# Kernel tuning notes

Measured on AMD Instinct MI355X. Metric: run time of the kernel, lower is better.

## Reference

```python
import jax, jax.numpy as jnp
import numpy as np

B, D, H, C = 512, 1024, 512, 4


def setup_inputs() -> dict:
    key = jax.random.key(0)
    k_x, k_v, k_w = jax.random.split(key, 3)
    # x holds categorical values in [0, C) used as float multipliers
    x = jax.random.randint(k_x, (B, D), 0, C).astype(jnp.float32)
    # xavier_normal_ per torch fan computation: V fan_in=D*C, fan_out=H*C; W fan_in=D, fan_out=H
    V = jax.random.normal(k_v, (H, D, C), jnp.float32) * np.float32(np.sqrt(2.0 / (D * C + H * C)))
    b = jnp.zeros((D, C), jnp.float32)
    W = jax.random.normal(k_w, (H, D), jnp.float32) * np.float32(np.sqrt(2.0 / (D + H)))
    c = jnp.zeros((1, H), jnp.float32)
    return {"x": x, "V": V, "b": b, "W": W, "c": c}


def _nade_forward(x, V, b, W, c):
    Bsz = x.shape[0]
    a0 = jnp.broadcast_to(c, (Bsz, c.shape[1]))  # [B, H]
    # per-step slices stacked along leading D axis for lax.scan
    xs = (jnp.transpose(V, (1, 0, 2)),  # [D, H, C]
          b,                            # [D, C]
          W.T,                          # [D, H]
          x.T)                          # [D, B]

    def step(a, inp):
        V_d, b_d, w_d, x_d = inp
        h = jax.nn.sigmoid(a)                 # [B, H]
        logits = h @ V_d + b_d                # [B, C]
        p = jax.nn.log_softmax(logits, axis=1)
        a_new = a + x_d[:, None] * w_d[None, :]  # rank-1 update of running preactivation
        return a_new, (logits, p)

    _, (logits, p) = jax.lax.scan(step, a0, xs)   # each [D, B, C]
    y_hat = jnp.transpose(logits, (1, 0, 2)).reshape(Bsz, -1)  # [B, D*C], d-major blocks of size C
    p_hat = jnp.transpose(p, (1, 0, 2)).reshape(Bsz, -1)
    return y_hat, p_hat


def reference(x, V, b, W, c):
    return _nade_forward(x, V, b, W, c)
```

## Files before the change

### kernel.cpp

```cpp
#include <hip/hip_runtime.h>


#define Bv 512
#define Dv 1024
#define Hv 512
#define Cv 4
#define Kv 32
#define DCv 32

#define L2E 1.4426950408889634f
#define LN2 0.6931471805599453f

typedef __attribute__((ext_vector_type(8))) short short8;
typedef __attribute__((ext_vector_type(4))) float f32x4;

__device__ __forceinline__ float fexp2(float x) { return __builtin_amdgcn_exp2f(x); }
__device__ __forceinline__ float flog2(float x) { return __builtin_amdgcn_logf(x); }
__device__ __forceinline__ float frcp(float x)  { return __builtin_amdgcn_rcpf(x); }

__device__ __forceinline__ unsigned bf16pk(float lo, float hi) {
    return __builtin_amdgcn_perm(__float_as_uint(hi), __float_as_uint(lo), 0x07060302u);
}
__device__ __forceinline__ unsigned short bf16rne(float f) {
    unsigned u = __float_as_uint(f);
    return (unsigned short)((u + 0x7FFFu + ((u >> 16) & 1u)) >> 16);
}

__global__ __launch_bounds__(256) void k_prep2(
        const float* __restrict__ W, const float* __restrict__ x,
        const float* __restrict__ V,
        float* __restrict__ WtL, float* __restrict__ xt,
        unsigned short* __restrict__ VtA4) {
    __shared__ __align__(16) char smem[16640];
    const int blk = blockIdx.x;

    if (blk < 1024) {
        unsigned short* tile = (unsigned short*)smem;
        const int d0 = (blk >> 2) * 4;
        const int hq = blk & 3;
        const int dd  = threadIdx.x & 3;
        const int hb0 = threadIdx.x >> 2;
#pragma unroll
        for (int p = 0; p < 2; ++p) {
            int h = hq * 128 + p * 64 + hb0;
            float4 v = *(const float4*)(V + ((size_t)h * Dv + d0 + dd) * Cv);
            int hbl = (h >> 5) - hq * 4;
            int q = (h >> 3) & 3, j = h & 7;
            int base = (dd * 4 + hbl) * 128 + q * 32 + j;
            tile[base + 0 * 8] = bf16rne(v.x);
            tile[base + 1 * 8] = bf16rne(v.y);
            tile[base + 2 * 8] = bf16rne(v.z);
            tile[base + 3 * 8] = bf16rne(v.w);
        }
        __syncthreads();
        {
            const uint4* srcp = (const uint4*)tile;
            int tt  = threadIdx.x;
            int dd2 = tt >> 6;
            int off = tt & 63;
            uint4* dst = (uint4*)VtA4;
            dst[(size_t)(d0 + dd2) * 256 + hq * 64 + off] = srcp[dd2 * 64 + off];
        }
    } else {
        float (*t)[65] = (float(*)[65])smem;
        const int t2   = blk - 1024;
        const int mb   = t2 >> 7;
        const int tile = t2 & 127;
        const int tr   = tile >> 4;
        const int tc   = tile & 15;
        const float* src = mb ? x : W;
        float* dst       = mb ? xt : WtL;
        const float scale = mb ? 1.0f : L2E;
        const int lx = threadIdx.x & 15;
        const int ly = threadIdx.x >> 4;
#pragma unroll
        for (int r = 0; r < 64; r += 16) {
            int row = r + ly;
            float4 v = *(const float4*)(src + (size_t)(tr * 64 + row) * Dv + tc * 64 + lx * 4);
            t[row][lx * 4 + 0] = v.x;
            t[row][lx * 4 + 1] = v.y;
            t[row][lx * 4 + 2] = v.z;
            t[row][lx * 4 + 3] = v.w;
        }
        __syncthreads();
#pragma unroll
        for (int r = 0; r < 64; r += 16) {
            int row = r + ly;
            float4 o = make_float4(t[lx * 4 + 0][row] * scale,
                                   t[lx * 4 + 1][row] * scale,
                                   t[lx * 4 + 2][row] * scale,
                                   t[lx * 4 + 3][row] * scale);
            *(float4*)(dst + (size_t)(tc * 64 + row) * 512 + tr * 64 + lx * 4) = o;
        }
    }
}

__global__ __launch_bounds__(512) void k_partial(const float* __restrict__ x,
                          const float* __restrict__ WtL, float* __restrict__ A0) {
    int k  = blockIdx.x >> 6;
    int bg = blockIdx.x & 63;
    int h  = threadIdx.x;
    int d0 = k * DCv;

    __shared__ float xs[DCv * 8];
    if (threadIdx.x < DCv * 8) {
        int g = threadIdx.x >> 5;
        int j = threadIdx.x & 31;
        xs[j * 8 + g] = x[(size_t)(bg * 8 + g) * Dv + d0 + j];
    }
    __syncthreads();

    float acc[8];
#pragma unroll
    for (int g = 0; g < 8; ++g) acc[g] = 0.0f;

    const float* wp = WtL + (size_t)d0 * Hv + h;
    for (int j = 0; j < DCv; ++j) {
        float wv = wp[(size_t)j * Hv];
        const float4 x0 = *(const float4*)(xs + j * 8);
        const float4 x1 = *(const float4*)(xs + j * 8 + 4);
        acc[0] = fmaf(x0.x, wv, acc[0]);
        acc[1] = fmaf(x0.y, wv, acc[1]);
        acc[2] = fmaf(x0.z, wv, acc[2]);
        acc[3] = fmaf(x0.w, wv, acc[3]);
        acc[4] = fmaf(x1.x, wv, acc[4]);
        acc[5] = fmaf(x1.y, wv, acc[5]);
        acc[6] = fmaf(x1.z, wv, acc[6]);
        acc[7] = fmaf(x1.w, wv, acc[7]);
    }
#pragma unroll
    for (int g = 0; g < 8; ++g)
        A0[((size_t)k * Bv + bg * 8 + g) * Hv + h] = acc[g];
}

__global__ void k_prefix(float* __restrict__ A0, const float* __restrict__ cbias) {
    int gid = blockIdx.x * blockDim.x + threadIdx.x;
    int h = gid & (Hv - 1);
    int bi = gid >> 9;
    float run = cbias[h] * L2E;
    float* p = A0 + (size_t)bi * Hv + h;
    for (int k = 0; k < Kv; ++k) {
        float t = p[(size_t)k * Bv * Hv];
        p[(size_t)k * Bv * Hv] = run;
        run += t;
    }
}

__global__ __launch_bounds__(256, 4) void k_main(
        const float* __restrict__ xt, const float* __restrict__ bbias,
        const unsigned short* __restrict__ VtA4, const float* __restrict__ WtL,
        const float* __restrict__ A0, float* __restrict__ out) {
    const int k    = blockIdx.x >> 5;
    const int bg   = blockIdx.x & 31;
    const int wid  = threadIdx.x >> 6;
    const int lane = threadIdx.x & 63;
    const int bl   = lane & 15;
    const int quad = lane >> 4;
    const int b    = bg * 16 + bl;
    const int d0   = k * DCv;

    __shared__ f32x4 red[2][8][4][16];

    float a[32];
    {
        const float* ap = A0 + ((size_t)k * Bv + b) * Hv + wid * 128 + quad * 8;
#pragma unroll
        for (int kb = 0; kb < 4; ++kb) {
            float4 t0 = *(const float4*)(ap + kb * 32);
            float4 t1 = *(const float4*)(ap + kb * 32 + 4);
            a[kb*8+0]=t0.x; a[kb*8+1]=t0.y; a[kb*8+2]=t0.z; a[kb*8+3]=t0.w;
            a[kb*8+4]=t1.x; a[kb*8+5]=t1.y; a[kb*8+6]=t1.z; a[kb*8+7]=t1.w;
        }
    }

    const bool act = (bl < 4);
    const unsigned short* vp = VtA4 + (((size_t)d0 * 16 + wid * 4) * 16 + quad * 4 + bl) * 8;
    const float* wp = WtL + (size_t)d0 * Hv + wid * 128 + quad * 8;
    const float* xp = xt + (size_t)d0 * Bv + b;

    const int  sE  = wid * 2 + (lane >> 5);
    const bool epi = ((lane >> 4) & 1) == 0;
    const float* bpE = bbias + (d0 + sE) * Cv;
    float* spY = out + (size_t)b * Dv * Cv + (d0 + sE) * Cv;
    float* spP = spY + (size_t)Bv * Dv * Cv;

    const short8 zfrag = {0,0,0,0,0,0,0,0};

    for (int i1 = 0; i1 < DCv / 8; ++i1) {
        const int buf = i1 & 1;
#pragma unroll 1
        for (int half = 0; half < 2; ++half) {
#pragma unroll
            for (int s = 0; s < 4; ++s) {
                short8 af[4];
#pragma unroll
                for (int kb = 0; kb < 4; ++kb)
                    af[kb] = act ? *(const short8*)(vp + s * 2048 + kb * 128) : zfrag;
                float xd = xp[s * Bv];

                unsigned pk[16];
#pragma unroll
                for (int m = 0; m < 32; m += 2) {
                    float s0 = frcp(1.0f + fexp2(-a[m]));
                    float s1 = frcp(1.0f + fexp2(-a[m + 1]));
                    pk[m >> 1] = bf16pk(s0, s1);
                }
                f32x4 acc = {0.f, 0.f, 0.f, 0.f};
#pragma unroll
                for (int kb = 0; kb < 4; ++kb) {
                    union { unsigned u[4]; short8 s8; } cv;
                    cv.u[0] = pk[kb*4+0]; cv.u[1] = pk[kb*4+1];
                    cv.u[2] = pk[kb*4+2]; cv.u[3] = pk[kb*4+3];
                    acc = __builtin_amdgcn_mfma_f32_16x16x32_bf16(af[kb], cv.s8, acc, 0, 0, 0);
                }
#pragma unroll
                for (int kb = 0; kb < 4; ++kb)
#pragma unroll
                    for (int j = 0; j < 8; ++j)
                        a[kb*8+j] = fmaf(xd, wp[s * Hv + kb*32 + j], a[kb*8+j]);

                if (quad == 0) red[buf][half * 4 + s][wid][bl] = acc;
            }
            vp += 4 * 2048;
            wp += 4 * Hv;
            xp += 4 * Bv;
        }
        __syncthreads();

        if (epi) {
            float4 bbv = *(const float4*)bpE;
            f32x4 r0 = red[buf][sE][0][bl];
            f32x4 r1 = red[buf][sE][1][bl];
            f32x4 r2 = red[buf][sE][2][bl];
            f32x4 r3 = red[buf][sE][3][bl];
            float w0 = r0.x + r1.x + r2.x + r3.x + bbv.x;
            float w1 = r0.y + r1.y + r2.y + r3.y + bbv.y;
            float w2 = r0.z + r1.z + r2.z + r3.z + bbv.z;
            float w3 = r0.w + r1.w + r2.w + r3.w + bbv.w;
            *(float4*)spY = make_float4(w0, w1, w2, w3);
            float mx = fmaxf(fmaxf(w0, w1), fmaxf(w2, w3));
            float e0 = fexp2((w0 - mx) * L2E);
            float e1 = fexp2((w1 - mx) * L2E);
            float e2 = fexp2((w2 - mx) * L2E);
            float e3 = fexp2((w3 - mx) * L2E);
            float lse = mx + flog2(e0 + e1 + e2 + e3) * LN2;
            *(float4*)spP = make_float4(w0 - lse, w1 - lse, w2 - lse, w3 - lse);
        }

        bpE += 8 * Cv;
        spY += 8 * Cv;
        spP += 8 * Cv;
    }
}

extern "C" void kernel_launch(void* const* d_in, const int* in_sizes, int n_in,
                              void* d_out, int out_size, void* d_ws, size_t ws_size,
                              hipStream_t stream) {
    const float* x  = (const float*)d_in[0];
    const float* V  = (const float*)d_in[1];
    const float* bb = (const float*)d_in[2];
    const float* W  = (const float*)d_in[3];
    const float* cb = (const float*)d_in[4];
    float* out = (float*)d_out;

    char* ws = (char*)d_ws;
    unsigned short* VtA4 = (unsigned short*)ws;
    float* WtL = (float*)(ws + (size_t)4 * 1024 * 1024);
    float* xt  = (float*)(ws + (size_t)6 * 1024 * 1024);
    float* A0  = (float*)(ws + (size_t)8 * 1024 * 1024);

    k_prep2<<<1280, 256, 0, stream>>>(W, x, V, WtL, xt, VtA4);
    k_partial<<<Kv * (Bv / 8), 512, 0, stream>>>(x, WtL, A0);
    k_prefix<<<(Bv * Hv) / 256, 256, 0, stream>>>(A0, cb);
    k_main<<<Kv * 32, 256, 0, stream>>>(xt, bb, VtA4, WtL, A0, out);
}
```

Measured before the change: 163.8 us.

## Fuse chunk partial sums and prefix scan into one kernel

Merges the per-chunk partial preactivation kernel and the separate prefix-scan kernel into a single kernel that walks all chunks sequentially per (b,h) and writes the running prefix directly. This removes one launch and the read-modify-write pass over A0 (32x512x512 floats) that the scan did. It reads W directly with an LDS-transposed tile instead of the pre-transposed WtL copy. In exchange, parallelism drops to 512 blocks each running a serial 32-step loop with two barriers per step.

```diff
diff --git a/kernel.cpp b/kernel.cpp
--- a/kernel.cpp
+++ b/kernel.cpp
@@ -95,54 +95,40 @@
     }
 }
 
-__global__ __launch_bounds__(512) void k_partial(const float* __restrict__ x,
-                          const float* __restrict__ WtL, float* __restrict__ A0) {
-    int k  = blockIdx.x >> 6;
-    int bg = blockIdx.x & 63;
-    int h  = threadIdx.x;
-    int d0 = k * DCv;
-
-    __shared__ float xs[DCv * 8];
-    if (threadIdx.x < DCv * 8) {
-        int g = threadIdx.x >> 5;
-        int j = threadIdx.x & 31;
-        xs[j * 8 + g] = x[(size_t)(bg * 8 + g) * Dv + d0 + j];
-    }
-    __syncthreads();
-
-    float acc[8];
-#pragma unroll
-    for (int g = 0; g < 8; ++g) acc[g] = 0.0f;
-
-    const float* wp = WtL + (size_t)d0 * Hv + h;
-    for (int j = 0; j < DCv; ++j) {
-        float wv = wp[(size_t)j * Hv];
-        const float4 x0 = *(const float4*)(xs + j * 8);
-        const float4 x1 = *(const float4*)(xs + j * 8 + 4);
-        acc[0] = fmaf(x0.x, wv, acc[0]);
-        acc[1] = fmaf(x0.y, wv, acc[1]);
-        acc[2] = fmaf(x0.z, wv, acc[2]);
-        acc[3] = fmaf(x0.w, wv, acc[3]);
-        acc[4] = fmaf(x1.x, wv, acc[4]);
-        acc[5] = fmaf(x1.y, wv, acc[5]);
-        acc[6] = fmaf(x1.z, wv, acc[6]);
-        acc[7] = fmaf(x1.w, wv, acc[7]);
-    }
-#pragma unroll
-    for (int g = 0; g < 8; ++g)
-        A0[((size_t)k * Bv + bg * 8 + g) * Hv + h] = acc[g];
-}
-
-__global__ void k_prefix(float* __restrict__ A0, const float* __restrict__ cbias) {
-    int gid = blockIdx.x * blockDim.x + threadIdx.x;
-    int h = gid & (Hv - 1);
-    int bi = gid >> 9;
+__global__ __launch_bounds__(512) void k_pp2(
+        const float* __restrict__ x, const float* __restrict__ W,
+        const float* __restrict__ cbias, float* __restrict__ A0) {
+    __shared__ float ws[64][33];
+    __shared__ float xs[32][8];
+    const int hg = blockIdx.x & 7;
+    const int bg = blockIdx.x >> 3;
+    const int h0 = hg * 64, b0 = bg * 8;
+    const int th = threadIdx.x & 63;
+    const int tb = threadIdx.x >> 6;
+    const int h = h0 + th, b = b0 + tb;
+
     float run = cbias[h] * L2E;
-    float* p = A0 + (size_t)bi * Hv + h;
+
     for (int k = 0; k < Kv; ++k) {
-        float t = p[(size_t)k * Bv * Hv];
-        p[(size_t)k * Bv * Hv] = run;
-        run += t;
+        const int d0 = k * DCv;
+        __syncthreads();
+#pragma unroll
+        for (int r = 0; r < 4; ++r) {
+            int idx = threadIdx.x + r * 512;
+            int i = idx >> 5, j = idx & 31;
+            ws[i][j] = W[(size_t)(h0 + i) * Dv + d0 + j] * L2E;
+        }
+        if (threadIdx.x < 256) {
+            int g = threadIdx.x >> 5, j = threadIdx.x & 31;
+            xs[j][g] = x[(size_t)(b0 + g) * Dv + d0 + j];
+        }
+        __syncthreads();
+        float acc = 0.0f;
+#pragma unroll
+        for (int j = 0; j < DCv; ++j)
+            acc = fmaf(xs[j][tb], ws[th][j], acc);
+        A0[(size_t)k * Bv * Hv + (size_t)b * Hv + h] = run;
+        run += acc;
     }
 }
 
@@ -270,7 +256,6 @@
     float* A0  = (float*)(ws + (size_t)8 * 1024 * 1024);
 
     k_prep2<<<1280, 256, 0, stream>>>(W, x, V, WtL, xt, VtA4);
-    k_partial<<<Kv * (Bv / 8), 512, 0, stream>>>(x, WtL, A0);
-    k_prefix<<<(Bv * Hv) / 256, 256, 0, stream>>>(A0, cb);
+    k_pp2<<<512, 512, 0, stream>>>(x, W, cb, A0);
     k_main<<<Kv * 32, 256, 0, stream>>>(xt, bb, VtA4, WtL, A0, out);
 }
```

Result: slower. 187.1 us (+14.2%).
